# Optimization experiments

Measured on AMD Instinct MI355X. Metric: run time of the kernel, lower is better.

## Reference

```python
import jax, jax.numpy as jnp
import numpy as np
from math import sqrt

CTX_LEN = 24
DK = 92
EMBED_DIM = 36
N_TOKENS = 500
HIDDEN = 152
CONCAT_DIM = 936  # 2*EMBED_DIM + EMBED_DIM*CTX_LEN


def setup_inputs() -> dict:
    key = jax.random.key(0)
    ks = jax.random.split(key, 12)
    u = lambda k, shp, s: jax.random.uniform(k, shp, dtype=jnp.float32) * s
    return {
        "x0": jax.random.normal(ks[0], (EMBED_DIM, CTX_LEN), dtype=jnp.float32),
        "wq1": u(ks[1], (CTX_LEN, DK), 0.05),
        "wk1": u(ks[2], (CTX_LEN, DK), 0.05),
        "wv1": u(ks[3], (CTX_LEN, DK), 0.05),
        "wq2": u(ks[4], (CTX_LEN, DK), 0.05),
        "wk2": u(ks[5], (CTX_LEN, DK), 0.05),
        "wv2": u(ks[6], (CTX_LEN, DK), 0.05),
        "nl0": u(ks[7], (CONCAT_DIM, HIDDEN), 0.05),
        "nl0_bias": u(ks[8], (HIDDEN,), 0.005),
        "nl1": u(ks[9], (HIDDEN, EMBED_DIM), 0.05),
        "ctp": u(ks[10], (EMBED_DIM, N_TOKENS), 0.05),
        "ctp_bias": u(ks[11], (N_TOKENS,), 0.005),
    }


def _self_attn(x, wq, wk, wv):
    # x: (E, C); wq/wk/wv: (C, DK)
    q = x @ wq
    k = x @ wk
    v = x @ wv
    # NOTE: original multiplies by sqrt(dk) (not divide) and softmaxes over dim 0
    scores = jax.nn.softmax((q @ k.T) * sqrt(DK), axis=0)  # (E, E)
    return scores @ v  # (E, DK)


def reference(x0, wq1, wk1, wv1, wq2, wk2, wv2, nl0, nl0_bias, nl1, ctp, ctp_bias):
    t3 = _self_attn(x0, wq1, wk1, wv1).sum(axis=1)   # (E,)
    t13 = _self_attn(x0, wq2, wk2, wv2).sum(axis=1)  # (E,)
    t71 = jnp.concatenate([t3, t13, x0.reshape(-1)])  # (936,)
    t7 = jax.nn.relu(t71 @ nl0) + nl0_bias            # (152,)
    t10 = t7 @ nl1                                    # (E,)
    return t10 @ ctp + ctp_bias                       # (N_TOKENS,)
```

## Files before the change

kernel.cpp:

```cpp
#include <hip/hip_runtime.h>
#include <math.h>

#define CTX 24
#define DKK 92
#define ED 36
#define NTOK 500
#define HID 152
#define CDIM 936

__global__ __launch_bounds__(256) void attn_kernel(
    const float* __restrict__ x0,
    const float* __restrict__ wq1, const float* __restrict__ wk1, const float* __restrict__ wv1,
    const float* __restrict__ wq2, const float* __restrict__ wk2, const float* __restrict__ wv2,
    float* __restrict__ t_out)
{
    const float* wq = blockIdx.x ? wq2 : wq1;
    const float* wk = blockIdx.x ? wk2 : wk1;
    const float* wv = blockIdx.x ? wv2 : wv1;
    float* dst = t_out + blockIdx.x * ED;

    __shared__ float x0s[ED * CTX];
    __shared__ float wqs[CTX * DKK];
    __shared__ float wks[CTX * DKK];
    __shared__ float W[CTX * CTX];
    __shared__ float M[ED * CTX];
    __shared__ float S[ED * ED];
    __shared__ float wvsum[CTX];
    __shared__ float vs2[ED];

    const int tid = threadIdx.x;

    for (int i = tid; i < ED * CTX; i += 256) x0s[i] = x0[i];
    for (int i = tid; i < CTX * DKK; i += 256) { wqs[i] = wq[i]; wks[i] = wk[i]; }
    if (tid < CTX) {
        float s = 0.f;
        for (int d = 0; d < DKK; ++d) s += wv[tid * DKK + d];
        wvsum[tid] = s;
    }
    __syncthreads();

    for (int i = tid; i < CTX * CTX; i += 256) {
        const int a = i / CTX, b = i % CTX;
        const float* qa = &wqs[a * DKK];
        const float* kb = &wks[b * DKK];
        float s = 0.f;
        for (int d = 0; d < DKK; ++d) s += qa[d] * kb[d];
        W[i] = s;
    }
    __syncthreads();

    for (int i = tid; i < ED * CTX; i += 256) {
        const int e = i / CTX, b = i % CTX;
        float s = 0.f;
        for (int a = 0; a < CTX; ++a) s += x0s[e * CTX + a] * W[a * CTX + b];
        M[i] = s;
    }
    __syncthreads();

    const float scale = sqrtf((float)DKK);
    for (int i = tid; i < ED * ED; i += 256) {
        const int e = i / ED, f = i % ED;
        float s = 0.f;
        for (int b = 0; b < CTX; ++b) s += M[e * CTX + b] * x0s[f * CTX + b];
        S[i] = s * scale;
    }
    __syncthreads();

    if (tid < ED) {
        const int f = tid;
        float mx = -1e30f;
        for (int e = 0; e < ED; ++e) mx = fmaxf(mx, S[e * ED + f]);
        float sum = 0.f;
        for (int e = 0; e < ED; ++e) {
            const float p = expf(S[e * ED + f] - mx);
            S[e * ED + f] = p;
            sum += p;
        }
        float vsum = 0.f;
        for (int c = 0; c < CTX; ++c) vsum += x0s[f * CTX + c] * wvsum[c];
        vs2[f] = vsum / sum;
    }
    __syncthreads();

    if (tid < ED) {
        const int e = tid;
        float s = 0.f;
        for (int f = 0; f < ED; ++f) s += S[e * ED + f] * vs2[f];
        dst[e] = s;
    }
}

#define JCHUNK 8
__global__ __launch_bounds__(256) void hidden_kernel(
    const float* __restrict__ x0, const float* __restrict__ nl0,
    const float* __restrict__ nl0_bias, const float* __restrict__ t36,
    float* __restrict__ h)
{
    __shared__ float t71[CDIM];
    __shared__ float part[32][JCHUNK];

    const int tid = threadIdx.x;
    for (int i = tid; i < 72; i += 256) t71[i] = t36[i];
    for (int i = tid; i < ED * CTX; i += 256) t71[72 + i] = x0[i];
    __syncthreads();

    const int isub = tid / JCHUNK;
    const int jj   = tid % JCHUNK;
    const int j    = blockIdx.x * JCHUNK + jj;

    float s = 0.f;
    for (int i = isub; i < CDIM; i += 32) s += t71[i] * nl0[i * HID + j];
    part[isub][jj] = s;
    __syncthreads();

    if (tid < JCHUNK) {
        float acc = 0.f;
        for (int k = 0; k < 32; ++k) acc += part[k][tid];
        const int jcol = blockIdx.x * JCHUNK + tid;
        h[jcol] = fmaxf(acc, 0.f) + nl0_bias[jcol];
    }
}

__global__ __launch_bounds__(512) void out_kernel(
    const float* __restrict__ h, const float* __restrict__ nl1,
    const float* __restrict__ ctp, const float* __restrict__ ctp_bias,
    float* __restrict__ out)
{
    __shared__ float hs[HID];
    __shared__ float t10[ED];

    const int tid = threadIdx.x;
    if (tid < HID) hs[tid] = h[tid];
    __syncthreads();

    if (tid < ED) {
        float s = 0.f;
        for (int j = 0; j < HID; ++j) s += hs[j] * nl1[j * ED + tid];
        t10[tid] = s;
    }
    __syncthreads();

    if (tid < NTOK) {
        float s = ctp_bias[tid];
        for (int e = 0; e < ED; ++e) s += t10[e] * ctp[e * NTOK + tid];
        out[tid] = s;
    }
}

extern "C" void kernel_launch(void* const* d_in, const int* in_sizes, int n_in,
                              void* d_out, int out_size, void* d_ws, size_t ws_size,
                              hipStream_t stream) {
    const float* x0       = (const float*)d_in[0];
    const float* wq1      = (const float*)d_in[1];
    const float* wk1      = (const float*)d_in[2];
    const float* wv1      = (const float*)d_in[3];
    const float* wq2      = (const float*)d_in[4];
    const float* wk2      = (const float*)d_in[5];
    const float* wv2      = (const float*)d_in[6];
    const float* nl0      = (const float*)d_in[7];
    const float* nl0_bias = (const float*)d_in[8];
    const float* nl1      = (const float*)d_in[9];
    const float* ctp      = (const float*)d_in[10];
    const float* ctp_bias = (const float*)d_in[11];

    float* ws = (float*)d_ws;

    attn_kernel<<<2, 256, 0, stream>>>(x0, wq1, wk1, wv1, wq2, wk2, wv2, ws);
    hidden_kernel<<<19, 256, 0, stream>>>(x0, nl0, nl0_bias, ws, ws + 72);
    out_kernel<<<1, 512, 0, stream>>>(ws + 72, nl1, ctp, ctp_bias, (float*)d_out);
}
```

Measured before the change: 25.30 us.

## Fuse attention, hidden and output stages into one single-block kernel

```diff
diff --git a/kernel.cpp b/kernel.cpp
--- a/kernel.cpp
+++ b/kernel.cpp
@@ -6,142 +6,212 @@
 #define ED 36
 #define NTOK 500
 #define HID 152
-#define CDIM 936
-
-__global__ __launch_bounds__(256) void attn_kernel(
+
+typedef float4 f4;
+
+__device__ __forceinline__ float dot4(f4 a, f4 b) {
+    return a.x*b.x + a.y*b.y + a.z*b.z + a.w*b.w;
+}
+
+struct AttnLds {
+    f4    xw4[216];
+    f4    W4[144];
+    f4    M4[216];
+    float S[1296];
+    float wvs[24];
+    f4    vs24[9];
+};
+
+__device__ void attn_wave(int lane, const float* __restrict__ x0,
+                          const float* __restrict__ wq, const float* __restrict__ wk,
+                          const float* __restrict__ wv,
+                          AttnLds& L, float* __restrict__ dst )
+{
+    const f4* x0g = (const f4*)x0;
+    for (int i = lane; i < 216; i += 64) L.xw4[i] = x0g[i];
+    if (lane < CTX) {
+        const f4* wvr = (const f4*)(wv + lane * DKK);
+        f4 s = {0.f, 0.f, 0.f, 0.f};
+        #pragma unroll
+        for (int c = 0; c < 23; ++c) {
+            f4 v = wvr[c];
+            s.x += v.x; s.y += v.y; s.z += v.z; s.w += v.w;
+        }
+        L.wvs[lane] = s.x + s.y + s.z + s.w;
+    }
+    __threadfence_block();
+
+    {
+        const f4* wq4 = (const f4*)wq;
+        const f4* wk4 = (const f4*)wk;
+        const int a0 = (lane >> 3) * 3, b0 = (lane & 7) * 3;
+        float acc[3][3] = {};
+        #pragma unroll 4
+        for (int dc = 0; dc < 23; ++dc) {
+            f4 qa[3], kb[3];
+            #pragma unroll
+            for (int r = 0; r < 3; ++r) qa[r] = wq4[(a0 + r) * 23 + dc];
+            #pragma unroll
+            for (int c = 0; c < 3; ++c) kb[c] = wk4[(b0 + c) * 23 + dc];
+            #pragma unroll
+            for (int r = 0; r < 3; ++r)
+                #pragma unroll
+                for (int c = 0; c < 3; ++c)
+                    acc[r][c] += dot4(qa[r], kb[c]);
+        }
+        float* Wf = (float*)L.W4;
+        #pragma unroll
+        for (int r = 0; r < 3; ++r)
+            #pragma unroll
+            for (int c = 0; c < 3; ++c)
+                Wf[(a0 + r) * 24 + b0 + c] = acc[r][c];
+    }
+    __threadfence_block();
+
+    {
+        const float* xf = (const float*)L.xw4;
+        for (int t = lane; t < 72; t += 64) {
+            const int e0 = (t / 6) * 3, bq = t % 6;
+            f4 acc[3] = {};
+            #pragma unroll
+            for (int a = 0; a < 24; ++a) {
+                f4 w = L.W4[a * 6 + bq];
+                #pragma unroll
+                for (int r = 0; r < 3; ++r) {
+                    float x = xf[(e0 + r) * 24 + a];
+                    acc[r].x += x * w.x; acc[r].y += x * w.y;
+                    acc[r].z += x * w.z; acc[r].w += x * w.w;
+                }
+            }
+            #pragma unroll
+            for (int r = 0; r < 3; ++r) L.M4[(e0 + r) * 6 + bq] = acc[r];
+        }
+    }
+    __threadfence_block();
+
+    {
+        const float scale = 9.59166304662544f;
+        for (int t = lane; t < 108; t += 64) {
+            const int e0 = (t / 9) * 3, f0 = (t % 9) * 4;
+            float acc[3][4] = {};
+            #pragma unroll
+            for (int bq = 0; bq < 6; ++bq) {
+                f4 m[3], x[4];
+                #pragma unroll
+                for (int r = 0; r < 3; ++r) m[r] = L.M4[(e0 + r) * 6 + bq];
+                #pragma unroll
+                for (int c = 0; c < 4; ++c) x[c] = L.xw4[(f0 + c) * 6 + bq];
+                #pragma unroll
+                for (int r = 0; r < 3; ++r)
+                    #pragma unroll
+                    for (int c = 0; c < 4; ++c)
+                        acc[r][c] += dot4(m[r], x[c]);
+            }
+            #pragma unroll
+            for (int r = 0; r < 3; ++r)
+                #pragma unroll
+                for (int c = 0; c < 4; ++c)
+                    L.S[(e0 + r) * 36 + f0 + c] = acc[r][c] * scale;
+        }
+    }
+    __threadfence_block();
+
+    if (lane < ED) {
+        const int f = lane;
+        float mx = -1e30f;
+        #pragma unroll 4
+        for (int e = 0; e < ED; ++e) mx = fmaxf(mx, L.S[e * 36 + f]);
+        float sum = 0.f;
+        #pragma unroll 4
+        for (int e = 0; e < ED; ++e) {
+            float p = expf(L.S[e * 36 + f] - mx);
+            L.S[e * 36 + f] = p;
+            sum += p;
+        }
+        const float* xf = (const float*)L.xw4;
+        float vs = 0.f;
+        #pragma unroll
+        for (int c = 0; c < CTX; ++c) vs += xf[f * 24 + c] * L.wvs[c];
+        ((float*)L.vs24)[f] = vs / sum;
+    }
+    __threadfence_block();
+
+    if (lane < ED) {
+        const int e = lane;
+        const f4* Srow = (const f4*)&L.S[e * 36];
+        float s = 0.f;
+        #pragma unroll
+        for (int fq = 0; fq < 9; ++fq) s += dot4(Srow[fq], L.vs24[fq]);
+        dst[e] = s;
+    }
+}
+
+#define NG 23
+__global__ __launch_bounds__(1024) void fused_kernel(
     const float* __restrict__ x0,
     const float* __restrict__ wq1, const float* __restrict__ wk1, const float* __restrict__ wv1,
     const float* __restrict__ wq2, const float* __restrict__ wk2, const float* __restrict__ wv2,
-    float* __restrict__ t_out)
-{
-    const float* wq = blockIdx.x ? wq2 : wq1;
-    const float* wk = blockIdx.x ? wk2 : wk1;
-    const float* wv = blockIdx.x ? wv2 : wv1;
-    float* dst = t_out + blockIdx.x * ED;
-
-    __shared__ float x0s[ED * CTX];
-    __shared__ float wqs[CTX * DKK];
-    __shared__ float wks[CTX * DKK];
-    __shared__ float W[CTX * CTX];
-    __shared__ float M[ED * CTX];
-    __shared__ float S[ED * ED];
-    __shared__ float wvsum[CTX];
-    __shared__ float vs2[ED];
-
-    const int tid = threadIdx.x;
-
-    for (int i = tid; i < ED * CTX; i += 256) x0s[i] = x0[i];
-    for (int i = tid; i < CTX * DKK; i += 256) { wqs[i] = wq[i]; wks[i] = wk[i]; }
-    if (tid < CTX) {
-        float s = 0.f;
-        for (int d = 0; d < DKK; ++d) s += wv[tid * DKK + d];
-        wvsum[tid] = s;
-    }
-    __syncthreads();
-
-    for (int i = tid; i < CTX * CTX; i += 256) {
-        const int a = i / CTX, b = i % CTX;
-        const float* qa = &wqs[a * DKK];
-        const float* kb = &wks[b * DKK];
-        float s = 0.f;
-        for (int d = 0; d < DKK; ++d) s += qa[d] * kb[d];
-        W[i] = s;
-    }
-    __syncthreads();
-
-    for (int i = tid; i < ED * CTX; i += 256) {
-        const int e = i / CTX, b = i % CTX;
-        float s = 0.f;
-        for (int a = 0; a < CTX; ++a) s += x0s[e * CTX + a] * W[a * CTX + b];
-        M[i] = s;
-    }
-    __syncthreads();
-
-    const float scale = sqrtf((float)DKK);
-    for (int i = tid; i < ED * ED; i += 256) {
-        const int e = i / ED, f = i % ED;
-        float s = 0.f;
-        for (int b = 0; b < CTX; ++b) s += M[e * CTX + b] * x0s[f * CTX + b];
-        S[i] = s * scale;
-    }
-    __syncthreads();
-
-    if (tid < ED) {
-        const int f = tid;
-        float mx = -1e30f;
-        for (int e = 0; e < ED; ++e) mx = fmaxf(mx, S[e * ED + f]);
-        float sum = 0.f;
-        for (int e = 0; e < ED; ++e) {
-            const float p = expf(S[e * ED + f] - mx);
-            S[e * ED + f] = p;
-            sum += p;
-        }
-        float vsum = 0.f;
-        for (int c = 0; c < CTX; ++c) vsum += x0s[f * CTX + c] * wvsum[c];
-        vs2[f] = vsum / sum;
-    }
-    __syncthreads();
-
-    if (tid < ED) {
-        const int e = tid;
-        float s = 0.f;
-        for (int f = 0; f < ED; ++f) s += S[e * ED + f] * vs2[f];
-        dst[e] = s;
-    }
-}
-
-#define JCHUNK 8
-__global__ __launch_bounds__(256) void hidden_kernel(
-    const float* __restrict__ x0, const float* __restrict__ nl0,
-    const float* __restrict__ nl0_bias, const float* __restrict__ t36,
-    float* __restrict__ h)
-{
-    __shared__ float t71[CDIM];
-    __shared__ float part[32][JCHUNK];
-
-    const int tid = threadIdx.x;
-    for (int i = tid; i < 72; i += 256) t71[i] = t36[i];
-    for (int i = tid; i < ED * CTX; i += 256) t71[72 + i] = x0[i];
-    __syncthreads();
-
-    const int isub = tid / JCHUNK;
-    const int jj   = tid % JCHUNK;
-    const int j    = blockIdx.x * JCHUNK + jj;
-
-    float s = 0.f;
-    for (int i = isub; i < CDIM; i += 32) s += t71[i] * nl0[i * HID + j];
-    part[isub][jj] = s;
-    __syncthreads();
-
-    if (tid < JCHUNK) {
-        float acc = 0.f;
-        for (int k = 0; k < 32; ++k) acc += part[k][tid];
-        const int jcol = blockIdx.x * JCHUNK + tid;
-        h[jcol] = fmaxf(acc, 0.f) + nl0_bias[jcol];
-    }
-}
-
-__global__ __launch_bounds__(512) void out_kernel(
-    const float* __restrict__ h, const float* __restrict__ nl1,
-    const float* __restrict__ ctp, const float* __restrict__ ctp_bias,
+    const float* __restrict__ nl0, const float* __restrict__ nl0_bias,
+    const float* __restrict__ nl1, const float* __restrict__ ctp, const float* __restrict__ ctp_bias,
     float* __restrict__ out)
 {
+    __shared__ AttnLds A0, A1;
+    __shared__ f4    part4[NG * 38];
+    __shared__ float conc72[72];
     __shared__ float hs[HID];
-    __shared__ float t10[ED];
+    __shared__ float t10p[144];
+    __shared__ f4    t10s4[9];
 
     const int tid = threadIdx.x;
-    if (tid < HID) hs[tid] = h[tid];
+
+    if (tid < 64) {
+        attn_wave(tid, x0, wq1, wk1, wv1, A0, conc72);
+    } else if (tid < 128) {
+        attn_wave(tid - 64, x0, wq2, wk2, wv2, A1, conc72 + ED);
+    } else if (tid < 128 + NG * 38) {
+        const int t = tid - 128;
+        const int g = t / 38, q = t % 38;
+        f4 acc = {0.f, 0.f, 0.f, 0.f};
+        const f4* nl04 = (const f4*)nl0;
+        #pragma unroll 4
+        for (int i = g; i < 864; i += NG) {
+            const float x = x0[i];
+            const f4 v = nl04[(72 + i) * 38 + q];
+            acc.x += x * v.x; acc.y += x * v.y; acc.z += x * v.z; acc.w += x * v.w;
+        }
+        part4[g * 38 + q] = acc;
+    }
+    __syncthreads();
+
+    if (tid < HID) {
+        const int j = tid;
+        const float* pf = (const float*)part4;
+        float s = 0.f;
+        #pragma unroll
+        for (int g = 0; g < NG; ++g) s += pf[g * 152 + j];
+        #pragma unroll 8
+        for (int i = 0; i < 72; ++i) s += conc72[i] * nl0[i * HID + j];
+        hs[j] = fmaxf(s, 0.f) + nl0_bias[j];
+    }
+    __syncthreads();
+
+    if (tid < 144) {
+        const int e = tid % 36, jg = tid / 36;
+        float s = 0.f;
+        for (int j = jg; j < HID; j += 4) s += hs[j] * nl1[j * 36 + e];
+        t10p[jg * 36 + e] = s;
+    }
     __syncthreads();
 
     if (tid < ED) {
-        float s = 0.f;
-        for (int j = 0; j < HID; ++j) s += hs[j] * nl1[j * ED + tid];
-        t10[tid] = s;
+        ((float*)t10s4)[tid] = t10p[tid] + t10p[36 + tid] + t10p[72 + tid] + t10p[108 + tid];
     }
     __syncthreads();
 
     if (tid < NTOK) {
+        const float* t10 = (const float*)t10s4;
         float s = ctp_bias[tid];
+        #pragma unroll
         for (int e = 0; e < ED; ++e) s += t10[e] * ctp[e * NTOK + tid];
         out[tid] = s;
     }
@@ -163,9 +233,7 @@
     const float* ctp      = (const float*)d_in[10];
     const float* ctp_bias = (const float*)d_in[11];
 
-    float* ws = (float*)d_ws;
-
-    attn_kernel<<<2, 256, 0, stream>>>(x0, wq1, wk1, wv1, wq2, wk2, wv2, ws);
-    hidden_kernel<<<19, 256, 0, stream>>>(x0, nl0, nl0_bias, ws, ws + 72);
-    out_kernel<<<1, 512, 0, stream>>>(ws + 72, nl1, ctp, ctp_bias, (float*)d_out);
-}
+    fused_kernel<<<1, 1024, 0, stream>>>(x0, wq1, wk1, wv1, wq2, wk2, wv2,
+                                         nl0, nl0_bias, nl1, ctp, ctp_bias,
+                                         (float*)d_out);
+}
```

Result: slower. 30.80 us (+21.7%).
